# Optimization experiments

Measured on AMD Instinct MI355X. Metric: run time of the kernel, lower is better.

## Reference

```python
import jax, jax.numpy as jnp
import numpy as np

N = 1000   # num_nodes
K = 4      # out-degree of regular random digraph
D = 256    # feature_dim
M = 4      # max_path_length


def _build_graph_and_paths():
    rng = np.random.default_rng(0)
    # K-regular random digraph: each node has exactly K distinct out-neighbors
    neigh = np.stack([rng.choice(N, size=K, replace=False) for _ in range(N)])  # [N,K]
    n = np.arange(N)
    p2 = np.stack([np.repeat(n, K), neigh.reshape(-1)], axis=1)                  # [N*K,2]
    p3 = np.concatenate([np.repeat(p2, K, axis=0), neigh[p2[:, 1]].reshape(-1, 1)], axis=1)
    p4 = np.concatenate([np.repeat(p3, K, axis=0), neigh[p3[:, 2]].reshape(-1, 1)], axis=1)
    pad = lambda p, L: np.pad(p, ((0, 0), (0, M - L)), constant_values=0)
    paths = np.concatenate([pad(p2, 2), pad(p3, 3), p4], axis=0).astype(np.int32)  # [84000,4]
    path_len = np.concatenate([np.full(len(p2), 2), np.full(len(p3), 3), np.full(len(p4), 4)]).astype(np.int32)
    return paths, path_len


def setup_inputs() -> dict:
    key = jax.random.key(0)
    ks = jax.random.split(key, 12)
    s = 0.05
    paths, path_len = _build_graph_and_paths()
    return {
        "node_features": jax.random.normal(ks[0], (N, D), dtype=jnp.float32),
        "paths": jnp.asarray(paths),
        "path_len": jnp.asarray(path_len),
        # per-step reasoning layers: Linear(2D->D), ReLU, Dropout(eval=identity), Linear(D->D)
        "W1": jax.random.normal(ks[1], (M - 1, 2 * D, D), dtype=jnp.float32) * s,
        "b1": jnp.zeros((M - 1, D), dtype=jnp.float32),
        "W2": jax.random.normal(ks[2], (M - 1, D, D), dtype=jnp.float32) * s,
        "b2": jnp.zeros((M - 1, D), dtype=jnp.float32),
        # path scorer: Linear(D->D//2), ReLU, Linear(D//2->1)
        "Ws1": jax.random.normal(ks[3], (D, D // 2), dtype=jnp.float32) * s,
        "bs1": jnp.zeros((D // 2,), dtype=jnp.float32),
        "Ws2": jax.random.normal(ks[4], (D // 2, 1), dtype=jnp.float32) * s,
        "bs2": jnp.zeros((1,), dtype=jnp.float32),
        # path aggregator: Linear(M*D->D), ReLU, Dropout(eval=identity), Linear(D->D)
        "Wa1": jax.random.normal(ks[5], (M * D, D), dtype=jnp.float32) * s,
        "ba1": jnp.zeros((D,), dtype=jnp.float32),
        "Wa2": jax.random.normal(ks[6], (D, D), dtype=jnp.float32) * s,
        "ba2": jnp.zeros((D,), dtype=jnp.float32),
    }


def reference(node_features, paths, path_len, W1, b1, W2, b2,
              Ws1, bs1, Ws2, bs2, Wa1, ba1, Wa2, ba2):
    # gather (current, next) node features for every hop of every path
    cur = node_features[paths[:, : M - 1]]          # [P, M-1, D]
    nxt = node_features[paths[:, 1:]]               # [P, M-1, D]
    cat = jnp.concatenate([cur, nxt], axis=-1)      # [P, M-1, 2D]
    # step-specific Linear(2D->D) -> ReLU -> Linear(D->D) (dropout = identity in eval)
    h = jax.nn.relu(jnp.einsum('psk,skd->psd', cat, W1) + b1)
    step = jnp.einsum('psd,sde->pse', h, W2) + b2   # [P, M-1, D]
    # mask out hops beyond each path's actual length
    mask = (jnp.arange(M - 1)[None, :] < (path_len[:, None] - 1)).astype(step.dtype)
    step = step * mask[..., None]
    P = paths.shape[0]
    feat = step.reshape(P, (M - 1) * D)
    feat = jnp.pad(feat, ((0, 0), (0, D)))          # zero-pad to M*D (aggregator input)
    # path scorer on first D dims (path confidences)
    scores = jax.nn.sigmoid(jax.nn.relu(feat[:, :D] @ Ws1 + bs1) @ Ws2 + bs2)  # [P,1]
    # aggregate path features and broadcast-add to every node
    agg = jax.nn.relu(feat @ Wa1 + ba1) @ Wa2 + ba2  # [P, D]
    aggregated = agg.sum(axis=0)                     # [D]
    updated = node_features + aggregated[None, :]
    return updated, scores
```

## Files before the change

### kernel.cpp

```cpp
#include <hip/hip_runtime.h>
#include <math.h>

typedef unsigned short ushort_t;
typedef __attribute__((ext_vector_type(8))) short short8;
typedef __attribute__((ext_vector_type(4))) float f32x4;

#define OFF_TREP  0u
#define OFF_P2    1048576u
#define OFF_SCE   1081344u
#define OFF_NFB   1097472u
#define OFF_W1T   1609472u
#define OFF_W2B   2395904u
#define OFF_WA1T  2789120u
#define OFF_WS1T  3182336u
#define OFF_UT    3247872u
#define OFF_VT    3641088u
#define OFF_C     3706624u
#define OFF_CS    3709696u
#define OFF_AB    3710208u
#define OFF_BB    6782208u
#define OFF_Z     9854208u

__device__ __forceinline__ ushort_t f2bf(float f) {
    unsigned u = __builtin_bit_cast(unsigned, f);
    return (ushort_t)((u + 0x7FFFu + ((u >> 16) & 1u)) >> 16);
}
__device__ __forceinline__ short8 ld8(const ushort_t* p) {
    return *(const short8*)(const void*)p;
}

__global__ __launch_bounds__(256) void k_pre(const float* __restrict__ nf,
                                             const float* __restrict__ W1,
                                             const float* __restrict__ W2,
                                             const float* __restrict__ Ws1,
                                             const float* __restrict__ b2,
                                             const float* __restrict__ Wa1,
                                             const float* __restrict__ bs1,
                                             char* __restrict__ ws) {
    ushort_t* nfb  = (ushort_t*)(ws + OFF_NFB);
    ushort_t* w1t  = (ushort_t*)(ws + OFF_W1T);
    ushort_t* w2b  = (ushort_t*)(ws + OFF_W2B);
    ushort_t* wa1t = (ushort_t*)(ws + OFF_WA1T);
    ushort_t* ws1t = (ushort_t*)(ws + OFF_WS1T);
    float*    cvec = (float*)(ws + OFF_C);
    float*    csv  = (float*)(ws + OFF_CS);
    __shared__ float tile[64][65];
    int t = threadIdx.x;
    int blk = blockIdx.x;
    if (blk < 152) {
        const float* src; ushort_t* dst; int src_ld, dst_ld;
        if (blk < 96) {
            int s = blk / 32, r = blk % 32, kt = r >> 2, dt = r & 3;
            src = W1 + s * 131072 + kt * 64 * 256 + dt * 64; src_ld = 256;
            dst = w1t + s * 131072 + dt * 64 * 512 + kt * 64; dst_ld = 512;
        } else if (blk < 144) {
            int t2 = blk - 96, s = t2 / 16, r = t2 % 16, kt = r >> 2, jt = r & 3;
            src = Wa1 + s * 65536 + kt * 64 * 256 + jt * 64; src_ld = 256;
            dst = wa1t + s * 65536 + jt * 64 * 256 + kt * 64; dst_ld = 256;
        } else {
            int t3 = blk - 144, kt = t3 >> 1, jt = t3 & 1;
            src = Ws1 + kt * 64 * 128 + jt * 64; src_ld = 128;
            dst = ws1t + jt * 64 * 256 + kt * 64; dst_ld = 256;
        }
        int lr = t >> 6, lc = t & 63;
#pragma unroll 4
        for (int r8 = 0; r8 < 16; r8++) {
            int row = r8 * 4 + lr;
            tile[row][lc] = src[row * src_ld + lc];
        }
        __syncthreads();
#pragma unroll 4
        for (int r8 = 0; r8 < 16; r8++) {
            int row = r8 * 4 + lr;
            dst[row * dst_ld + lc] = f2bf(tile[lc][row]);
        }
    } else if (blk < 408) {
        for (int i = (blk - 152) * 256 + t; i < 452608; i += 65536) {
            if (i < 256000) nfb[i] = f2bf(nf[i]);
            else            w2b[i - 256000] = f2bf(W2[i - 256000]);
        }
    } else if (blk < 411) {
        int s = blk - 408;
        const float* wp = Wa1 + s * 65536 + t;
        const float* bp = b2 + s * 256;
        float acc = 0.f;
        for (int k = 0; k < 256; k++) acc = fmaf(bp[k], wp[k * 256], acc);
        cvec[s * 256 + t] = acc;
    } else if (t < 128) {
        float acc = bs1[t];
        for (int k = 0; k < 256; k++) acc = fmaf(b2[k], Ws1[k * 128 + t], acc);
        csv[t] = acc;
    }
}

__global__ __launch_bounds__(256) void k_gemm(const float* __restrict__ b1,
                                              char* __restrict__ ws) {
    ushort_t* nfb  = (ushort_t*)(ws + OFF_NFB);
    ushort_t* w1t  = (ushort_t*)(ws + OFF_W1T);
    ushort_t* w2b  = (ushort_t*)(ws + OFF_W2B);
    ushort_t* wa1t = (ushort_t*)(ws + OFF_WA1T);
    ushort_t* ws1t = (ushort_t*)(ws + OFF_WS1T);
    ushort_t* Ut   = (ushort_t*)(ws + OFF_UT);
    ushort_t* Vt   = (ushort_t*)(ws + OFF_VT);
    float*    Ab   = (float*)(ws + OFF_AB);
    float*    Bb   = (float*)(ws + OFF_BB);

    int t = threadIdx.x;
    int task = blockIdx.x;
    int wid = t >> 6, lane = t & 63;
    int lane15 = lane & 15, kb = lane >> 4;
    const ushort_t *Abase, *Bbase;
    int ldb, rowbase, colbase, maxrow, mode, s = 0;
    float* Cf = nullptr; ushort_t* Cb = nullptr;
    if (task < 384) {
        s = task / 128; int rem = task % 128;
        int rb = rem >> 3, cb = rem & 7;
        int half = cb >> 2, cbl = cb & 3;
        rowbase = rb * 64 + wid * 16; colbase = cbl * 64; maxrow = 1000;
        Abase = nfb; Bbase = w1t + s * 131072 + half * 256; ldb = 512;
        Cf = (half ? Bb : Ab) + s * 256000; mode = half ? 1 : 0;
    } else if (task < 432) {
        int t2 = task - 384;
        s = t2 >> 4; int rem = t2 & 15;
        rowbase = (rem >> 2) * 64 + wid * 16; colbase = (rem & 3) * 64; maxrow = 256;
        Abase = wa1t + s * 65536; Bbase = w2b + s * 65536; ldb = 256;
        Cb = Ut + s * 65536; mode = 2;
    } else {
        int t3 = task - 432;
        rowbase = (t3 >> 2) * 64 + wid * 16; colbase = (t3 & 3) * 64; maxrow = 128;
        Abase = ws1t; Bbase = w2b; ldb = 256;
        Cb = Vt; mode = 2;
    }
    int lrow = min(rowbase + lane15, maxrow - 1);
    const ushort_t* ap = Abase + lrow * 256 + kb * 8;
    const ushort_t* bp = Bbase + (colbase + lane15) * ldb + kb * 8;
    f32x4 acc[4] = {};
#pragma unroll
    for (int k0 = 0; k0 < 8; k0++) {
        short8 af = ld8(ap + k0 * 32);
#pragma unroll
        for (int ct = 0; ct < 4; ct++)
            acc[ct] = __builtin_amdgcn_mfma_f32_16x16x32_bf16(
                af, ld8(bp + ct * 16 * ldb + k0 * 32), acc[ct], 0, 0, 0);
    }
    int rb2 = rowbase + kb * 4;
#pragma unroll
    for (int ct = 0; ct < 4; ct++) {
        int col = colbase + ct * 16 + lane15;
        float bias = (mode == 0) ? b1[s * 256 + col] : 0.f;
#pragma unroll
        for (int r = 0; r < 4; r++) {
            int row = rb2 + r;
            if (row < maxrow) {
                if (mode <= 1) Cf[row * 256 + col] = acc[ct][r] + bias;
                else           Cb[row * 256 + col] = f2bf(acc[ct][r]);
            }
        }
    }
}

__global__ __launch_bounds__(256, 4) void k_hz(const int* __restrict__ paths,
                                               const float* __restrict__ Ws2,
                                               const float* __restrict__ bs2,
                                               char* __restrict__ ws) {
    const float* Ab = (const float*)(ws + OFF_AB);
    const float* Bb = (const float*)(ws + OFF_BB);
    const ushort_t* Ut = (const ushort_t*)(ws + OFF_UT);
    const ushort_t* Vt = (const ushort_t*)(ws + OFF_VT);
    const float* csv = (const float*)(ws + OFF_CS);
    float* Z   = (float*)(ws + OFF_Z);
    float* sce = (float*)(ws + OFF_SCE);

    int task = blockIdx.x;
    int t = threadIdx.x;
    int wid = t >> 6, lane = t & 63;
    int lane15 = lane & 15, kb = lane >> 4;
    int s, rb, cb, iscore;
    if (task < 756) { s = task / 252; int rem = task % 252; rb = rem >> 2; cb = rem & 3; iscore = 0; }
    else            { s = 0; rb = task - 756; cb = 0; iscore = 1; }

    int rowbase = rb * 64 + wid * 16;
    int erow = min(rowbase + lane15, 3999);
    int src = erow >> 2;
    int dst = paths[erow * 4 + 1];
    const float* ap = Ab + (s * 1000 + src) * 256 + kb * 8;
    const float* bp = Bb + (s * 1000 + dst) * 256 + kb * 8;

    short8 hfrag[8];
#pragma unroll
    for (int k0 = 0; k0 < 8; k0++) {
        f32x4 a0 = *(const f32x4*)(ap + k0 * 32);
        f32x4 a1 = *(const f32x4*)(ap + k0 * 32 + 4);
        f32x4 c0 = *(const f32x4*)(bp + k0 * 32);
        f32x4 c1 = *(const f32x4*)(bp + k0 * 32 + 4);
        short8 hf;
#pragma unroll
        for (int j = 0; j < 4; j++) hf[j]     = (short)f2bf(fmaxf(a0[j] + c0[j], 0.f));
#pragma unroll
        for (int j = 0; j < 4; j++) hf[j + 4] = (short)f2bf(fmaxf(a1[j] + c1[j], 0.f));
        hfrag[k0] = hf;
    }

    int rb2 = rowbase + kb * 4;
    if (!iscore) {
        const ushort_t* up = Ut + s * 65536 + (cb * 64 + lane15) * 256 + kb * 8;
        f32x4 acc[4] = {};
#pragma unroll
        for (int k0 = 0; k0 < 8; k0++) {
            short8 af = hfrag[k0];
#pragma unroll
            for (int ct = 0; ct < 4; ct++)
                acc[ct] = __builtin_amdgcn_mfma_f32_16x16x32_bf16(
                    af, ld8(up + ct * 4096 + k0 * 32), acc[ct], 0, 0, 0);
        }
#pragma unroll
        for (int ct = 0; ct < 4; ct++) {
            int col = cb * 64 + ct * 16 + lane15;
#pragma unroll
            for (int r = 0; r < 4; r++) {
                int row = rb2 + r;
                if (row < 4000) Z[(s * 4000 + row) * 256 + col] = acc[ct][r];
            }
        }
    } else {
        const ushort_t* vp = Vt + lane15 * 256 + kb * 8;
        f32x4 acc2[8] = {};
#pragma unroll
        for (int k0 = 0; k0 < 8; k0++) {
            short8 af = hfrag[k0];
#pragma unroll
            for (int ct = 0; ct < 8; ct++)
                acc2[ct] = __builtin_amdgcn_mfma_f32_16x16x32_bf16(
                    af, ld8(vp + ct * 4096 + k0 * 32), acc2[ct], 0, 0, 0);
        }
        float w2v[8], cv[8];
#pragma unroll
        for (int ct = 0; ct < 8; ct++) {
            int col = ct * 16 + lane15;
            w2v[ct] = Ws2[col]; cv[ct] = csv[col];
        }
        float bb = bs2[0];
#pragma unroll
        for (int r = 0; r < 4; r++) {
            float y = 0.f;
#pragma unroll
            for (int ct = 0; ct < 8; ct++) y += fmaxf(acc2[ct][r] + cv[ct], 0.f) * w2v[ct];
            y += __shfl_xor(y, 1, 64); y += __shfl_xor(y, 2, 64);
            y += __shfl_xor(y, 4, 64); y += __shfl_xor(y, 8, 64);
            int row = rb2 + r;
            if (lane15 == 0 && row < 4000)
                sce[row] = 1.f / (1.f + expf(-(y + bb)));
        }
    }
}

__global__ __launch_bounds__(256) void k_path(const int* __restrict__ paths,
                                              const float* __restrict__ ba1,
                                              char* __restrict__ ws,
                                              float* __restrict__ out) {
    const float* Z    = (const float*)(ws + OFF_Z);
    const float* cvec = (const float*)(ws + OFF_C);
    const float* sce  = (const float*)(ws + OFF_SCE);
    float* Trep = (float*)(ws + OFF_TREP);
    int t = threadIdx.x;
    float zb2 = ba1[t] + cvec[t];
    float zb3 = zb2 + cvec[256 + t];
    float zb4 = zb3 + cvec[512 + t];
    const float* Z0 = Z;
    const float* Z1 = Z + 1024000;
    const float* Z2 = Z + 2048000;
    float acc = 0.f;
    for (int b = blockIdx.x; b < 4000; b += 1024) {
        float z0 = Z0[b * 256 + t];
        acc += fmaxf(zb2 + z0, 0.f);
#pragma unroll
        for (int j = 0; j < 4; j++) {
            int q = b * 4 + j;
            int n1 = paths[(4000 + q) * 4 + 1];
            float w = z0 + Z1[(n1 * 4 + j) * 256 + t];
            acc += fmaxf(zb3 + w, 0.f);
            int n2 = paths[(4000 + q) * 4 + 2];
            const float* z2p = Z2 + n2 * 1024 + t;
            acc += fmaxf(zb4 + w + z2p[0],   0.f);
            acc += fmaxf(zb4 + w + z2p[256], 0.f);
            acc += fmaxf(zb4 + w + z2p[512], 0.f);
            acc += fmaxf(zb4 + w + z2p[768], 0.f);
        }
    }
    Trep[blockIdx.x * 256 + t] = acc;
    int p = blockIdx.x * 256 + t;
    if (p < 84000) {
        int e0 = p < 4000 ? p : (p < 20000 ? ((p - 4000) >> 2) : ((p - 20000) >> 4));
        out[256000 + p] = sce[e0];
    }
}

__global__ __launch_bounds__(256) void k_agg(const float* __restrict__ Wa2,
                                             char* __restrict__ ws) {
    const float* Trep = (const float*)(ws + OFF_TREP);
    float* part2 = (float*)(ws + OFF_P2);
    __shared__ float tl[256];
    int t = threadIdx.x, i = blockIdx.x;
    float ts = 0.f;
#pragma unroll 8
    for (int r = 0; r < 32; r++) ts += Trep[(i * 32 + r) * 256 + t];
    tl[t] = ts;
    __syncthreads();
    float acc = 0.f;
    for (int k = 0; k < 256; k++) acc = fmaf(tl[k], Wa2[k * 256 + t], acc);
    part2[i * 256 + t] = acc;
}

__global__ __launch_bounds__(256) void k_fin(const float* __restrict__ nf,
                                             const float* __restrict__ ba2,
                                             char* __restrict__ ws,
                                             float* __restrict__ out) {
    const float* part2 = (const float*)(ws + OFF_P2);
    int t = threadIdx.x;
    float a = 84000.f * ba2[t];
#pragma unroll 8
    for (int r = 0; r < 32; r++) a += part2[r * 256 + t];
    int idx = blockIdx.x * 256 + t;
    out[idx] = nf[idx] + a;
}

extern "C" void kernel_launch(void* const* d_in, const int* in_sizes, int n_in,
                              void* d_out, int out_size, void* d_ws, size_t ws_size,
                              hipStream_t stream) {
    const float* nf    = (const float*)d_in[0];
    const int*   paths = (const int*)d_in[1];
    const float* W1    = (const float*)d_in[3];
    const float* b1    = (const float*)d_in[4];
    const float* W2    = (const float*)d_in[5];
    const float* b2    = (const float*)d_in[6];
    const float* Ws1   = (const float*)d_in[7];
    const float* bs1   = (const float*)d_in[8];
    const float* Ws2   = (const float*)d_in[9];
    const float* bs2   = (const float*)d_in[10];
    const float* Wa1   = (const float*)d_in[11];
    const float* ba1   = (const float*)d_in[12];
    const float* Wa2   = (const float*)d_in[13];
    const float* ba2   = (const float*)d_in[14];
    char* ws = (char*)d_ws;
    float* out = (float*)d_out;

    k_pre <<<412, 256, 0, stream>>>(nf, W1, W2, Ws1, b2, Wa1, bs1, ws);
    k_gemm<<<440, 256, 0, stream>>>(b1, ws);
    k_hz  <<<819, 256, 0, stream>>>(paths, Ws2, bs2, ws);
    k_path<<<1024, 256, 0, stream>>>(paths, ba1, ws, out);
    k_agg <<<32, 256, 0, stream>>>(Wa2, ws);
    k_fin <<<1000, 256, 0, stream>>>(nf, ba2, ws, out);
}
```

Measured before the change: 158.6 us.

## Fuse bf16 preprocessing into GEMM, store Z as bf16, atomic aggregation

Removes the separate k_pre kernel: each GEMM block now converts its fp32 operands to bf16 itself, staging the transposed weight tile in shared memory. The Z intermediate is stored as bf16 instead of fp32, halving the gather traffic in k_path at some precision cost. k_agg accumulates into a single vector with atomicAdd (zeroed by a memset), and k_fin becomes a vectorized float4 kernel with fewer blocks. This trades one launch and the bf16 staging buffers for redundant per-block conversions and strided fp32 weight reads.

```diff
diff --git a/kernel.cpp b/kernel.cpp
--- a/kernel.cpp
+++ b/kernel.cpp
@@ -5,157 +5,146 @@
 typedef __attribute__((ext_vector_type(8))) short short8;
 typedef __attribute__((ext_vector_type(4))) float f32x4;
 
-#define OFF_TREP  0u
-#define OFF_P2    1048576u
-#define OFF_SCE   1081344u
-#define OFF_NFB   1097472u
-#define OFF_W1T   1609472u
-#define OFF_W2B   2395904u
-#define OFF_WA1T  2789120u
-#define OFF_WS1T  3182336u
-#define OFF_UT    3247872u
-#define OFF_VT    3641088u
-#define OFF_C     3706624u
-#define OFF_CS    3709696u
-#define OFF_AB    3710208u
-#define OFF_BB    6782208u
-#define OFF_Z     9854208u
+#define OFF_TREP 0u
+#define OFF_AGG  1048576u
+#define OFF_SCE  1049600u
+#define OFF_UT   1065600u
+#define OFF_VT   1458816u
+#define OFF_C    1524352u
+#define OFF_CS   1527424u
+#define OFF_AB   1527936u
+#define OFF_BB   4599936u
+#define OFF_Z    7671936u
 
 __device__ __forceinline__ ushort_t f2bf(float f) {
     unsigned u = __builtin_bit_cast(unsigned, f);
     return (ushort_t)((u + 0x7FFFu + ((u >> 16) & 1u)) >> 16);
 }
+__device__ __forceinline__ float bf2f(ushort_t u) {
+    unsigned v = ((unsigned)u) << 16;
+    return __builtin_bit_cast(float, v);
+}
 __device__ __forceinline__ short8 ld8(const ushort_t* p) {
     return *(const short8*)(const void*)p;
 }
-
-__global__ __launch_bounds__(256) void k_pre(const float* __restrict__ nf,
-                                             const float* __restrict__ W1,
-                                             const float* __restrict__ W2,
-                                             const float* __restrict__ Ws1,
-                                             const float* __restrict__ b2,
-                                             const float* __restrict__ Wa1,
-                                             const float* __restrict__ bs1,
-                                             char* __restrict__ ws) {
-    ushort_t* nfb  = (ushort_t*)(ws + OFF_NFB);
-    ushort_t* w1t  = (ushort_t*)(ws + OFF_W1T);
-    ushort_t* w2b  = (ushort_t*)(ws + OFF_W2B);
-    ushort_t* wa1t = (ushort_t*)(ws + OFF_WA1T);
-    ushort_t* ws1t = (ushort_t*)(ws + OFF_WS1T);
+__device__ __forceinline__ short8 cvt8(f32x4 a, f32x4 b) {
+    short8 r;
+#pragma unroll
+    for (int j = 0; j < 4; j++) { r[j] = (short)f2bf(a[j]); r[j + 4] = (short)f2bf(b[j]); }
+    return r;
+}
+
+__global__ __launch_bounds__(256) void k_gemm(const float* __restrict__ nf,
+                                              const float* __restrict__ W1,
+                                              const float* __restrict__ b1,
+                                              const float* __restrict__ W2,
+                                              const float* __restrict__ b2,
+                                              const float* __restrict__ Ws1,
+                                              const float* __restrict__ bs1,
+                                              const float* __restrict__ Wa1,
+                                              char* __restrict__ ws) {
+    ushort_t* Ut   = (ushort_t*)(ws + OFF_UT);
+    ushort_t* Vt   = (ushort_t*)(ws + OFF_VT);
     float*    cvec = (float*)(ws + OFF_C);
     float*    csv  = (float*)(ws + OFF_CS);
-    __shared__ float tile[64][65];
-    int t = threadIdx.x;
-    int blk = blockIdx.x;
-    if (blk < 152) {
-        const float* src; ushort_t* dst; int src_ld, dst_ld;
-        if (blk < 96) {
-            int s = blk / 32, r = blk % 32, kt = r >> 2, dt = r & 3;
-            src = W1 + s * 131072 + kt * 64 * 256 + dt * 64; src_ld = 256;
-            dst = w1t + s * 131072 + dt * 64 * 512 + kt * 64; dst_ld = 512;
-        } else if (blk < 144) {
-            int t2 = blk - 96, s = t2 / 16, r = t2 % 16, kt = r >> 2, jt = r & 3;
-            src = Wa1 + s * 65536 + kt * 64 * 256 + jt * 64; src_ld = 256;
-            dst = wa1t + s * 65536 + jt * 64 * 256 + kt * 64; dst_ld = 256;
+    float*    Ab   = (float*)(ws + OFF_AB);
+    float*    Bb   = (float*)(ws + OFF_BB);
+    __shared__ ushort_t blds[64][264];
+    int t = threadIdx.x, task = blockIdx.x;
+    int wid = t >> 6, lane = t & 63;
+    int lane15 = lane & 15, kb = lane >> 4;
+
+    if (task < 384) {
+        int s = task / 128, rem = task % 128;
+        int rb = rem >> 3, cb8 = rem & 7, half = cb8 >> 2, cbl = cb8 & 3;
+        const float* w1p = W1 + s * 131072 + half * 65536 + cbl * 64;
+        {
+            int dl = t & 63, kq = t >> 6;
+            for (int i = 0; i < 64; i++) {
+                int k = i * 4 + kq;
+                blds[dl][k] = f2bf(w1p[k * 256 + dl]);
+            }
+        }
+        __syncthreads();
+        int rowbase = rb * 64 + wid * 16;
+        int lrow = min(rowbase + lane15, 999);
+        const float* ap = nf + lrow * 256 + kb * 8;
+        f32x4 acc[4] = {};
+#pragma unroll
+        for (int k0 = 0; k0 < 8; k0++) {
+            f32x4 a0 = *(const f32x4*)(ap + k0 * 32);
+            f32x4 a1 = *(const f32x4*)(ap + k0 * 32 + 4);
+            short8 af = cvt8(a0, a1);
+#pragma unroll
+            for (int ct = 0; ct < 4; ct++)
+                acc[ct] = __builtin_amdgcn_mfma_f32_16x16x32_bf16(
+                    af, ld8(&blds[ct * 16 + lane15][kb * 8 + k0 * 32]), acc[ct], 0, 0, 0);
+        }
+        float* Cf = (half ? Bb : Ab) + s * 256000;
+        int rb2 = rowbase + kb * 4;
+#pragma unroll
+        for (int ct = 0; ct < 4; ct++) {
+            int col = cbl * 64 + ct * 16 + lane15;
+            float bias = half ? 0.f : b1[s * 256 + col];
+#pragma unroll
+            for (int r = 0; r < 4; r++) {
+                int row = rb2 + r;
+                if (row < 1000) Cf[row * 256 + col] = acc[ct][r] + bias;
+            }
+        }
+    } else if (task < 440) {
+        const float* Asrc; const float* Bsrc; ushort_t* Cout;
+        int a_ld, rb0, colbase;
+        if (task < 432) {
+            int t2 = task - 384, s = t2 >> 4, rem = t2 & 15;
+            rb0 = (rem >> 2) * 64; colbase = (rem & 3) * 64;
+            Asrc = Wa1 + s * 65536; a_ld = 256;
+            Bsrc = W2 + s * 65536;  Cout = Ut + s * 65536;
         } else {
-            int t3 = blk - 144, kt = t3 >> 1, jt = t3 & 1;
-            src = Ws1 + kt * 64 * 128 + jt * 64; src_ld = 128;
-            dst = ws1t + jt * 64 * 256 + kt * 64; dst_ld = 256;
-        }
-        int lr = t >> 6, lc = t & 63;
-#pragma unroll 4
-        for (int r8 = 0; r8 < 16; r8++) {
-            int row = r8 * 4 + lr;
-            tile[row][lc] = src[row * src_ld + lc];
+            int t3 = task - 432;
+            rb0 = (t3 >> 2) * 64; colbase = (t3 & 3) * 64;
+            Asrc = Ws1; a_ld = 128;
+            Bsrc = W2;  Cout = Vt;
+        }
+        {
+            int el = t & 63, eq = t >> 6;
+            for (int i = 0; i < 64; i++) {
+                int e = i * 4 + eq;
+                blds[el][e] = f2bf(Asrc[e * a_ld + rb0 + el]);
+            }
         }
         __syncthreads();
-#pragma unroll 4
-        for (int r8 = 0; r8 < 16; r8++) {
-            int row = r8 * 4 + lr;
-            dst[row * dst_ld + lc] = f2bf(tile[lc][row]);
-        }
-    } else if (blk < 408) {
-        for (int i = (blk - 152) * 256 + t; i < 452608; i += 65536) {
-            if (i < 256000) nfb[i] = f2bf(nf[i]);
-            else            w2b[i - 256000] = f2bf(W2[i - 256000]);
-        }
-    } else if (blk < 411) {
-        int s = blk - 408;
-        const float* wp = Wa1 + s * 65536 + t;
-        const float* bp = b2 + s * 256;
+        int rowloc = wid * 16 + lane15;
+        f32x4 acc[4] = {};
+#pragma unroll
+        for (int k0 = 0; k0 < 8; k0++) {
+            short8 af = ld8(&blds[rowloc][kb * 8 + k0 * 32]);
+#pragma unroll
+            for (int ct = 0; ct < 4; ct++) {
+                const float* bp = Bsrc + (colbase + ct * 16 + lane15) * 256 + kb * 8 + k0 * 32;
+                f32x4 b0 = *(const f32x4*)bp;
+                f32x4 b1v = *(const f32x4*)(bp + 4);
+                acc[ct] = __builtin_amdgcn_mfma_f32_16x16x32_bf16(
+                    af, cvt8(b0, b1v), acc[ct], 0, 0, 0);
+            }
+        }
+        int rowg = rb0 + wid * 16 + kb * 4;
+#pragma unroll
+        for (int ct = 0; ct < 4; ct++) {
+            int col = colbase + ct * 16 + lane15;
+#pragma unroll
+            for (int r = 0; r < 4; r++)
+                Cout[(rowg + r) * 256 + col] = f2bf(acc[ct][r]);
+        }
+    } else if (task < 443) {
+        int s = task - 440;
         float acc = 0.f;
-        for (int k = 0; k < 256; k++) acc = fmaf(bp[k], wp[k * 256], acc);
+        for (int k = 0; k < 256; k++) acc = fmaf(b2[s * 256 + k], Wa1[(s * 256 + k) * 256 + t], acc);
         cvec[s * 256 + t] = acc;
     } else if (t < 128) {
         float acc = bs1[t];
         for (int k = 0; k < 256; k++) acc = fmaf(b2[k], Ws1[k * 128 + t], acc);
         csv[t] = acc;
-    }
-}
-
-__global__ __launch_bounds__(256) void k_gemm(const float* __restrict__ b1,
-                                              char* __restrict__ ws) {
-    ushort_t* nfb  = (ushort_t*)(ws + OFF_NFB);
-    ushort_t* w1t  = (ushort_t*)(ws + OFF_W1T);
-    ushort_t* w2b  = (ushort_t*)(ws + OFF_W2B);
-    ushort_t* wa1t = (ushort_t*)(ws + OFF_WA1T);
-    ushort_t* ws1t = (ushort_t*)(ws + OFF_WS1T);
-    ushort_t* Ut   = (ushort_t*)(ws + OFF_UT);
-    ushort_t* Vt   = (ushort_t*)(ws + OFF_VT);
-    float*    Ab   = (float*)(ws + OFF_AB);
-    float*    Bb   = (float*)(ws + OFF_BB);
-
-    int t = threadIdx.x;
-    int task = blockIdx.x;
-    int wid = t >> 6, lane = t & 63;
-    int lane15 = lane & 15, kb = lane >> 4;
-    const ushort_t *Abase, *Bbase;
-    int ldb, rowbase, colbase, maxrow, mode, s = 0;
-    float* Cf = nullptr; ushort_t* Cb = nullptr;
-    if (task < 384) {
-        s = task / 128; int rem = task % 128;
-        int rb = rem >> 3, cb = rem & 7;
-        int half = cb >> 2, cbl = cb & 3;
-        rowbase = rb * 64 + wid * 16; colbase = cbl * 64; maxrow = 1000;
-        Abase = nfb; Bbase = w1t + s * 131072 + half * 256; ldb = 512;
-        Cf = (half ? Bb : Ab) + s * 256000; mode = half ? 1 : 0;
-    } else if (task < 432) {
-        int t2 = task - 384;
-        s = t2 >> 4; int rem = t2 & 15;
-        rowbase = (rem >> 2) * 64 + wid * 16; colbase = (rem & 3) * 64; maxrow = 256;
-        Abase = wa1t + s * 65536; Bbase = w2b + s * 65536; ldb = 256;
-        Cb = Ut + s * 65536; mode = 2;
-    } else {
-        int t3 = task - 432;
-        rowbase = (t3 >> 2) * 64 + wid * 16; colbase = (t3 & 3) * 64; maxrow = 128;
-        Abase = ws1t; Bbase = w2b; ldb = 256;
-        Cb = Vt; mode = 2;
-    }
-    int lrow = min(rowbase + lane15, maxrow - 1);
-    const ushort_t* ap = Abase + lrow * 256 + kb * 8;
-    const ushort_t* bp = Bbase + (colbase + lane15) * ldb + kb * 8;
-    f32x4 acc[4] = {};
-#pragma unroll
-    for (int k0 = 0; k0 < 8; k0++) {
-        short8 af = ld8(ap + k0 * 32);
-#pragma unroll
-        for (int ct = 0; ct < 4; ct++)
-            acc[ct] = __builtin_amdgcn_mfma_f32_16x16x32_bf16(
-                af, ld8(bp + ct * 16 * ldb + k0 * 32), acc[ct], 0, 0, 0);
-    }
-    int rb2 = rowbase + kb * 4;
-#pragma unroll
-    for (int ct = 0; ct < 4; ct++) {
-        int col = colbase + ct * 16 + lane15;
-        float bias = (mode == 0) ? b1[s * 256 + col] : 0.f;
-#pragma unroll
-        for (int r = 0; r < 4; r++) {
-            int row = rb2 + r;
-            if (row < maxrow) {
-                if (mode <= 1) Cf[row * 256 + col] = acc[ct][r] + bias;
-                else           Cb[row * 256 + col] = f2bf(acc[ct][r]);
-            }
-        }
     }
 }
 
@@ -168,7 +157,7 @@
     const ushort_t* Ut = (const ushort_t*)(ws + OFF_UT);
     const ushort_t* Vt = (const ushort_t*)(ws + OFF_VT);
     const float* csv = (const float*)(ws + OFF_CS);
-    float* Z   = (float*)(ws + OFF_Z);
+    ushort_t* Zb = (ushort_t*)(ws + OFF_Z);
     float* sce = (float*)(ws + OFF_SCE);
 
     int task = blockIdx.x;
@@ -219,7 +208,7 @@
 #pragma unroll
             for (int r = 0; r < 4; r++) {
                 int row = rb2 + r;
-                if (row < 4000) Z[(s * 4000 + row) * 256 + col] = acc[ct][r];
+                if (row < 4000) Zb[(s * 4000 + row) * 256 + col] = f2bf(acc[ct][r]);
             }
         }
     } else {
@@ -258,33 +247,33 @@
                                               const float* __restrict__ ba1,
                                               char* __restrict__ ws,
                                               float* __restrict__ out) {
-    const float* Z    = (const float*)(ws + OFF_Z);
-    const float* cvec = (const float*)(ws + OFF_C);
-    const float* sce  = (const float*)(ws + OFF_SCE);
+    const ushort_t* Zb = (const ushort_t*)(ws + OFF_Z);
+    const float* cvec  = (const float*)(ws + OFF_C);
+    const float* sce   = (const float*)(ws + OFF_SCE);
     float* Trep = (float*)(ws + OFF_TREP);
     int t = threadIdx.x;
     float zb2 = ba1[t] + cvec[t];
     float zb3 = zb2 + cvec[256 + t];
     float zb4 = zb3 + cvec[512 + t];
-    const float* Z0 = Z;
-    const float* Z1 = Z + 1024000;
-    const float* Z2 = Z + 2048000;
+    const ushort_t* Z0 = Zb;
+    const ushort_t* Z1 = Zb + 1024000;
+    const ushort_t* Z2 = Zb + 2048000;
     float acc = 0.f;
     for (int b = blockIdx.x; b < 4000; b += 1024) {
-        float z0 = Z0[b * 256 + t];
+        float z0 = bf2f(Z0[b * 256 + t]);
         acc += fmaxf(zb2 + z0, 0.f);
 #pragma unroll
         for (int j = 0; j < 4; j++) {
             int q = b * 4 + j;
             int n1 = paths[(4000 + q) * 4 + 1];
-            float w = z0 + Z1[(n1 * 4 + j) * 256 + t];
+            float w = z0 + bf2f(Z1[(n1 * 4 + j) * 256 + t]);
             acc += fmaxf(zb3 + w, 0.f);
             int n2 = paths[(4000 + q) * 4 + 2];
-            const float* z2p = Z2 + n2 * 1024 + t;
-            acc += fmaxf(zb4 + w + z2p[0],   0.f);
-            acc += fmaxf(zb4 + w + z2p[256], 0.f);
-            acc += fmaxf(zb4 + w + z2p[512], 0.f);
-            acc += fmaxf(zb4 + w + z2p[768], 0.f);
+            const ushort_t* z2p = Z2 + n2 * 1024 + t;
+            acc += fmaxf(zb4 + w + bf2f(z2p[0]),   0.f);
+            acc += fmaxf(zb4 + w + bf2f(z2p[256]), 0.f);
+            acc += fmaxf(zb4 + w + bf2f(z2p[512]), 0.f);
+            acc += fmaxf(zb4 + w + bf2f(z2p[768]), 0.f);
         }
     }
     Trep[blockIdx.x * 256 + t] = acc;
@@ -298,7 +287,7 @@
 __global__ __launch_bounds__(256) void k_agg(const float* __restrict__ Wa2,
                                              char* __restrict__ ws) {
     const float* Trep = (const float*)(ws + OFF_TREP);
-    float* part2 = (float*)(ws + OFF_P2);
+    float* agg = (float*)(ws + OFF_AGG);
     __shared__ float tl[256];
     int t = threadIdx.x, i = blockIdx.x;
     float ts = 0.f;
@@ -308,20 +297,22 @@
     __syncthreads();
     float acc = 0.f;
     for (int k = 0; k < 256; k++) acc = fmaf(tl[k], Wa2[k * 256 + t], acc);
-    part2[i * 256 + t] = acc;
+    atomicAdd(&agg[t], acc);
 }
 
 __global__ __launch_bounds__(256) void k_fin(const float* __restrict__ nf,
                                              const float* __restrict__ ba2,
                                              char* __restrict__ ws,
                                              float* __restrict__ out) {
-    const float* part2 = (const float*)(ws + OFF_P2);
-    int t = threadIdx.x;
-    float a = 84000.f * ba2[t];
-#pragma unroll 8
-    for (int r = 0; r < 32; r++) a += part2[r * 256 + t];
-    int idx = blockIdx.x * 256 + t;
-    out[idx] = nf[idx] + a;
+    const float* agg = (const float*)(ws + OFF_AGG);
+    int gid = blockIdx.x * 256 + threadIdx.x;
+    int d0 = (gid * 4) & 255;
+    f32x4 x = *(const f32x4*)(nf + gid * 4);
+    f32x4 a = *(const f32x4*)(agg + d0);
+    f32x4 b = *(const f32x4*)(ba2 + d0);
+#pragma unroll
+    for (int j = 0; j < 4; j++) x[j] += a[j] + 84000.f * b[j];
+    *(f32x4*)(out + gid * 4) = x;
 }
 
 extern "C" void kernel_launch(void* const* d_in, const int* in_sizes, int n_in,
@@ -344,10 +335,10 @@
     char* ws = (char*)d_ws;
     float* out = (float*)d_out;
 
-    k_pre <<<412, 256, 0, stream>>>(nf, W1, W2, Ws1, b2, Wa1, bs1, ws);
-    k_gemm<<<440, 256, 0, stream>>>(b1, ws);
+    hipMemsetAsync(ws + OFF_AGG, 0, 1024, stream);
+    k_gemm<<<444, 256, 0, stream>>>(nf, W1, b1, W2, b2, Ws1, bs1, Wa1, ws);
     k_hz  <<<819, 256, 0, stream>>>(paths, Ws2, bs2, ws);
     k_path<<<1024, 256, 0, stream>>>(paths, ba1, ws, out);
     k_agg <<<32, 256, 0, stream>>>(Wa2, ws);
-    k_fin <<<1000, 256, 0, stream>>>(nf, ba2, ws, out);
-}
+    k_fin <<<250, 256, 0, stream>>>(nf, ba2, ws, out);
+}
```

Result: faster. 146.4 us (-7.7%).
